# Optimization experiments

Hardware: AMD Instinct MI355X
Metric: run time of the kernel (lower is better)

## Reference

```python
import jax, jax.numpy as jnp
import numpy as np

EPS = 1e-5  # BatchNorm eps


def _conv_bn_tanh(h, w, b, g, be, m, v):
    # 3x3 conv, stride 1, SAME padding (pad = k//2), NCHW / OIHW
    y = jax.lax.conv_general_dilated(
        h, w, window_strides=(1, 1), padding='SAME',
        dimension_numbers=('NCHW', 'OIHW', 'NCHW'))
    y = y + b[None, :, None, None]
    # BatchNorm inference: gamma * (y - mean) / sqrt(var + eps) + beta
    scale = g * jax.lax.rsqrt(v + EPS)
    y = y * scale[None, :, None, None] + (be - m * scale)[None, :, None, None]
    return jnp.tanh(y)


def _unfold3x3(x):
    # torch F.unfold(k=3, pad=1, stride=1) -> (N, C, 9, H, W), kernel positions row-major
    N, C, H, W = x.shape
    xp = jnp.pad(x, ((0, 0), (0, 0), (1, 1), (1, 1)))
    patches = [xp[:, :, i:i + H, j:j + W] for i in range(3) for j in range(3)]
    return jnp.stack(patches, axis=2)  # (N, C, 9, H, W)


def setup_inputs() -> dict:
    key = jax.random.key(0)
    ks = jax.random.split(key, 24)
    N, C, H, W = 8, 64, 128, 128
    INTER, FEAT, NB, KK = 64, 6, 6, 9
    d = {}
    d['x'] = jax.random.normal(ks[0], (N, C, H, W), jnp.float32)
    d['w0'] = jax.random.normal(ks[1], (INTER, C, 3, 3), jnp.float32) * 0.05
    d['b0'] = jax.random.normal(ks[2], (INTER,), jnp.float32) * 0.05
    d['g0'] = jax.random.uniform(ks[3], (INTER,), jnp.float32)
    d['be0'] = jax.random.normal(ks[4], (INTER,), jnp.float32) * 0.05
    d['m0'] = jax.random.normal(ks[5], (INTER,), jnp.float32) * 0.05
    d['v0'] = jax.random.uniform(ks[6], (INTER,), jnp.float32)
    d['wm'] = jax.random.normal(ks[7], (5, INTER, INTER, 3, 3), jnp.float32) * 0.05
    d['bm'] = jax.random.normal(ks[8], (5, INTER), jnp.float32) * 0.05
    d['gm'] = jax.random.uniform(ks[9], (5, INTER), jnp.float32)
    d['bem'] = jax.random.normal(ks[10], (5, INTER), jnp.float32) * 0.05
    d['mm'] = jax.random.normal(ks[11], (5, INTER), jnp.float32) * 0.05
    d['vm'] = jax.random.uniform(ks[12], (5, INTER), jnp.float32)
    OC = FEAT * NB  # 36
    d['wl'] = jax.random.normal(ks[13], (OC, INTER, 3, 3), jnp.float32) * 0.05
    d['bl'] = jax.random.normal(ks[14], (OC,), jnp.float32) * 0.05
    d['gl'] = jax.random.uniform(ks[15], (OC,), jnp.float32)
    d['bel'] = jax.random.normal(ks[16], (OC,), jnp.float32) * 0.05
    d['ml'] = jax.random.normal(ks[17], (OC,), jnp.float32) * 0.05
    d['vl'] = jax.random.uniform(ks[18], (OC,), jnp.float32)
    d['bases'] = jax.random.normal(ks[19], (NB, KK), jnp.float32)  # FB bases buffer (6, 9)
    return d


def reference(x, w0, b0, g0, be0, m0, v0, wm, bm, gm, bem, mm, vm,
              wl, bl, gl, bel, ml, vl, bases):
    N, C, H, W = x.shape
    FEAT, NB = 6, 6
    # bases_net: conv-bn-tanh x7 (eval mode, dropout no-ops)
    h = _conv_bn_tanh(x, w0, b0, g0, be0, m0, v0)
    for i in range(5):
        h = _conv_bn_tanh(h, wm[i], bm[i], gm[i], bem[i], mm[i], vm[i])
    h = _conv_bn_tanh(h, wl, bl, gl, bel, ml, vl)  # (N, 36, H, W)
    bfeat = h.reshape(N, FEAT, NB, H, W)
    # per-pixel basis coefficients: (N, M, 9, H, W)
    bcoef = jnp.einsum('bmkhw,kl->bmlhw', bfeat, bases)
    patches = _unfold3x3(x)  # (N, C, 9, H, W)
    # dynamic conv: combine per-pixel coeffs with unfolded input
    out = jnp.einsum('bmlhw,bclhw->bcmhw', bcoef, patches)  # (N, C, M, H, W)
    return out.reshape(N, C * NB, H, W)
```

## Files before the change

kernel.cpp:

```cpp
#include <hip/hip_runtime.h>
#include <hip/hip_bf16.h>

typedef short bf16x4 __attribute__((ext_vector_type(4)));
typedef short bf16x8 __attribute__((ext_vector_type(8)));
typedef float f32x4  __attribute__((ext_vector_type(4)));

__device__ inline unsigned short f2us(float f) {
    __hip_bfloat16 h = __float2bfloat16(f);
    return *(unsigned short*)&h;
}
__device__ inline float us2f(unsigned short u) {
    union { unsigned int i; float f; } c; c.i = ((unsigned int)u) << 16; return c.f;
}
__device__ inline float tanh_fast(float x) {
    float xs = fminf(fmaxf(x, -20.f), 20.f);
    float t = __expf(2.f * xs);
    return 1.f - 2.f / (t + 1.f);
}

__global__ __launch_bounds__(256) void prep_x(const float* __restrict__ x,
                                              unsigned short* __restrict__ xcl)
{
    __shared__ unsigned short t2[128 * 68];
    int bid = blockIdx.x;
    int n = bid >> 7, h = bid & 127;
    const float* xp = x + (size_t)n * 64 * 16384 + h * 128;
    int t = threadIdx.x;
    for (int i = t; i < 8192; i += 256) {
        int ci = i >> 7, w = i & 127;
        t2[w * 68 + ci] = f2us(xp[(size_t)ci * 16384 + w]);
    }
    __syncthreads();
    unsigned short* op = xcl + ((size_t)(n * 16384 + h * 128)) * 64;
    for (int i = t; i < 1024; i += 256) {
        int w = i >> 3, c8 = i & 7;
        union { bf16x4 v[2]; uint4 q; } u;
        u.v[0] = *(bf16x4*)&t2[w * 68 + c8 * 8];
        u.v[1] = *(bf16x4*)&t2[w * 68 + c8 * 8 + 4];
        *(uint4*)(op + w * 64 + c8 * 8) = u.q;
    }
}

__global__ void prep_wf(const float* __restrict__ w0, const float* __restrict__ wm,
                        const float* __restrict__ wl, unsigned short* __restrict__ Wf)
{
    int idx = blockIdx.x * 256 + threadIdx.x;
    if (idx >= 258048) return;
    int l = idx / 36864, r = idx - l * 36864;
    int tp = r >> 12, r2 = r & 4095;
    int hh = r2 >> 11, nb = (r2 >> 9) & 3, ln = (r2 >> 3) & 63, j = r2 & 7;
    int ci = hh * 32 + (ln >> 4) * 8 + j;
    int co = nb * 16 + (ln & 15);
    float val = 0.f;
    if (l < 6) {
        const float* src = (l == 0) ? w0 : (wm + (size_t)(l - 1) * 36864);
        val = src[(co * 64 + ci) * 9 + tp];
    } else if (co < 36) {
        val = wl[(co * 64 + ci) * 9 + tp];
    }
    Wf[idx] = f2us(val);
}

__global__ void prep_ab(const float* b0, const float* g0, const float* be0,
                        const float* m0, const float* v0,
                        const float* bm, const float* gm, const float* bem,
                        const float* mm, const float* vm,
                        const float* bl, const float* gl, const float* bel,
                        const float* ml, const float* vl,
                        float* __restrict__ Af, float* __restrict__ Bf)
{
    int idx = blockIdx.x * 256 + threadIdx.x;
    if (idx >= 448) return;
    int l = idx >> 6, c = idx & 63;
    float b, g, be, m, v;
    if (l == 0) {
        b = b0[c]; g = g0[c]; be = be0[c]; m = m0[c]; v = v0[c];
    } else if (l < 6) {
        int o = (l - 1) * 64 + c;
        b = bm[o]; g = gm[o]; be = bem[o]; m = mm[o]; v = vm[o];
    } else {
        if (c >= 36) { Af[idx] = 0.f; Bf[idx] = 0.f; return; }
        b = bl[c]; g = gl[c]; be = bel[c]; m = ml[c]; v = vl[c];
    }
    float s = g / sqrtf(v + 1e-5f);
    Af[idx] = s;
    Bf[idx] = (b - m) * s + be;
}

__global__ __launch_bounds__(256)
void conv_mfma(const unsigned short* __restrict__ src,
               const unsigned short* __restrict__ Wf,
               const float* __restrict__ A, const float* __restrict__ B,
               unsigned short* __restrict__ dst)
{
    __shared__ unsigned short tile[18 * 18 * 68];
    const int n = blockIdx.z;
    const int h0 = blockIdx.y * 16, w0 = blockIdx.x * 16;
    const int t = threadIdx.x;
    const size_t ibase = (size_t)n * 16384 * 64;

    for (int i = t; i < 5184; i += 256) {
        int p = i >> 4, c4 = i & 15;
        int ty = p / 18, tx = p - ty * 18;
        int gy = h0 + ty - 1, gx = w0 + tx - 1;
        uint2 v = make_uint2(0u, 0u);
        if ((unsigned)gy < 128u && (unsigned)gx < 128u)
            v = *(const uint2*)(src + ibase + (size_t)(gy * 128 + gx) * 64 + c4 * 4);
        *(uint2*)&tile[p * 68 + c4 * 4] = v;
    }
    __syncthreads();

    const int ln = t & 63, wv = t >> 6;
    const int xln = ln & 15, qd = ln >> 4;

    f32x4 acc[4][4];
#pragma unroll
    for (int mt = 0; mt < 4; ++mt)
#pragma unroll
        for (int nb = 0; nb < 4; ++nb)
            acc[mt][nb] = (f32x4){0.f, 0.f, 0.f, 0.f};

    const uint4* wf4 = (const uint4*)Wf;
#pragma unroll
    for (int tp = 0; tp < 9; ++tp) {
        const int ky = tp / 3, kx = tp % 3;
        bf16x8 b[2][4];
#pragma unroll
        for (int hh = 0; hh < 2; ++hh)
#pragma unroll
            for (int nb = 0; nb < 4; ++nb) {
                uint4 q = wf4[((tp * 2 + hh) * 4 + nb) * 64 + ln];
                b[hh][nb] = *(bf16x8*)&q;
            }
#pragma unroll
        for (int mt = 0; mt < 4; ++mt) {
            const int off0 = ((wv * 4 + mt + ky) * 18 + xln + kx) * 68 + qd * 8;
#pragma unroll
            for (int hh = 0; hh < 2; ++hh) {
                union { bf16x8 v8; bf16x4 v4[2]; } a;
                a.v4[0] = *(const bf16x4*)&tile[off0 + hh * 32];
                a.v4[1] = *(const bf16x4*)&tile[off0 + hh * 32 + 4];
#pragma unroll
                for (int nb = 0; nb < 4; ++nb)
                    acc[mt][nb] = __builtin_amdgcn_mfma_f32_16x16x32_bf16(
                        a.v8, b[hh][nb], acc[mt][nb], 0, 0, 0);
            }
        }
    }

#pragma unroll
    for (int mt = 0; mt < 4; ++mt) {
        const int gy = h0 + wv * 4 + mt;
        unsigned short* dp = dst + ibase + (size_t)(gy * 128) * 64;
#pragma unroll
        for (int nb = 0; nb < 4; ++nb) {
            const int co = nb * 16 + xln;
            const float As = A[co], Bs = B[co];
#pragma unroll
            for (int r = 0; r < 4; ++r) {
                const int gx = w0 + qd * 4 + r;
                float y = tanh_fast(fmaf(acc[mt][nb][r], As, Bs));
                dp[(size_t)gx * 64 + co] = f2us(y);
            }
        }
    }
}

__global__ __launch_bounds__(256)
void dyn_conv(const float* __restrict__ x, const unsigned short* __restrict__ h7,
              const float* __restrict__ bases, float* __restrict__ out)
{
    __shared__ float tile[32 * 10 * 34];
    const int n = blockIdx.z;
    const int h0 = blockIdx.y * 8, w0 = blockIdx.x * 32;
    const float* xp = x + (size_t)n * 64 * 16384;
    const int t = threadIdx.x;
    const int tw = t & 31, th = t >> 5;
    const int h = h0 + th, w = w0 + tw;

    float bs[54];
#pragma unroll
    for (int i = 0; i < 54; ++i) bs[i] = bases[i];

    union { uint4 q[5]; unsigned short s[40]; } hv;
    const unsigned short* hp = h7 + (size_t)(n * 16384 + h * 128 + w) * 64;
#pragma unroll
    for (int i = 0; i < 5; ++i) hv.q[i] = ((const uint4*)hp)[i];

    float coef[54];
#pragma unroll
    for (int i = 0; i < 54; ++i) coef[i] = 0.f;
#pragma unroll
    for (int m = 0; m < 6; ++m)
#pragma unroll
        for (int k = 0; k < 6; ++k) {
            float f = us2f(hv.s[m * 6 + k]);
#pragma unroll
            for (int l = 0; l < 9; ++l)
                coef[m * 9 + l] = fmaf(f, bs[k * 9 + l], coef[m * 9 + l]);
        }

    float* op = out + (size_t)n * 384 * 16384 + h * 128 + w;

    for (int half = 0; half < 2; ++half) {
        if (half) __syncthreads();
        for (int idx = t; idx < 32 * 340; idx += 256) {
            int ci = idx / 340, r = idx % 340, y = r / 34, xw = r % 34;
            int gy = h0 + y - 1, gx = w0 + xw - 1;
            float v = 0.f;
            if ((unsigned)gy < 128u && (unsigned)gx < 128u)
                v = xp[(size_t)(half * 32 + ci) * 16384 + gy * 128 + gx];
            tile[idx] = v;
        }
        __syncthreads();

#pragma unroll 1
        for (int c = 0; c < 32; ++c) {
            float xv[9];
#pragma unroll
            for (int ky = 0; ky < 3; ++ky)
#pragma unroll
                for (int kx = 0; kx < 3; ++kx)
                    xv[ky * 3 + kx] = tile[c * 340 + (th + ky) * 34 + (tw + kx)];
            int cg = half * 32 + c;
#pragma unroll
            for (int m = 0; m < 6; ++m) {
                float s = 0.f;
#pragma unroll
                for (int l = 0; l < 9; ++l) s = fmaf(coef[m * 9 + l], xv[l], s);
                op[(size_t)(cg * 6 + m) * 16384] = s;
            }
        }
    }
}

extern "C" void kernel_launch(void* const* d_in, const int* in_sizes, int n_in,
                              void* d_out, int out_size, void* d_ws, size_t ws_size,
                              hipStream_t stream)
{
    const float* x   = (const float*)d_in[0];
    const float* w0  = (const float*)d_in[1];
    const float* b0  = (const float*)d_in[2];
    const float* g0  = (const float*)d_in[3];
    const float* be0 = (const float*)d_in[4];
    const float* m0  = (const float*)d_in[5];
    const float* v0  = (const float*)d_in[6];
    const float* wm  = (const float*)d_in[7];
    const float* bm  = (const float*)d_in[8];
    const float* gm  = (const float*)d_in[9];
    const float* bem = (const float*)d_in[10];
    const float* mm  = (const float*)d_in[11];
    const float* vm  = (const float*)d_in[12];
    const float* wl  = (const float*)d_in[13];
    const float* bl  = (const float*)d_in[14];
    const float* gl  = (const float*)d_in[15];
    const float* bel = (const float*)d_in[16];
    const float* ml  = (const float*)d_in[17];
    const float* vl  = (const float*)d_in[18];
    const float* bas = (const float*)d_in[19];

    unsigned short* Wfb = (unsigned short*)d_ws;
    float* Af  = (float*)((char*)d_ws + 524288);
    float* Bf  = Af + 448;
    unsigned short* xcl  = (unsigned short*)((char*)d_ws + (size_t)(2  << 20));
    unsigned short* bufA = (unsigned short*)((char*)d_ws + (size_t)(2  << 20) + 16777216);
    unsigned short* bufB = (unsigned short*)((char*)d_ws + (size_t)(2  << 20) + 2 * 16777216);

    prep_x<<<1024, 256, 0, stream>>>(x, xcl);
    prep_wf<<<1008, 256, 0, stream>>>(w0, wm, wl, Wfb);
    prep_ab<<<2, 256, 0, stream>>>(b0, g0, be0, m0, v0,
                                   bm, gm, bem, mm, vm,
                                   bl, gl, bel, ml, vl, Af, Bf);

    dim3 cg(8, 8, 8);
    conv_mfma<<<cg, 256, 0, stream>>>(xcl,  Wfb + 0 * 36864, Af + 0,   Bf + 0,   bufA);
    conv_mfma<<<cg, 256, 0, stream>>>(bufA, Wfb + 1 * 36864, Af + 64,  Bf + 64,  bufB);
    conv_mfma<<<cg, 256, 0, stream>>>(bufB, Wfb + 2 * 36864, Af + 128, Bf + 128, bufA);
    conv_mfma<<<cg, 256, 0, stream>>>(bufA, Wfb + 3 * 36864, Af + 192, Bf + 192, bufB);
    conv_mfma<<<cg, 256, 0, stream>>>(bufB, Wfb + 4 * 36864, Af + 256, Bf + 256, bufA);
    conv_mfma<<<cg, 256, 0, stream>>>(bufA, Wfb + 5 * 36864, Af + 320, Bf + 320, bufB);
    conv_mfma<<<cg, 256, 0, stream>>>(bufB, Wfb + 6 * 36864, Af + 384, Bf + 384, bufA);

    dim3 dg(4, 16, 8);
    dyn_conv<<<dg, 256, 0, stream>>>(x, bufA, bas, (float*)d_out);
}
```

Before: 500.7 us.

## Stage conv tiles and weights in LDS via direct global-to-LDS loads

The conv kernel now runs 512-thread blocks on 16x32 output tiles. The haloed input tile and all 3x3 weight fragments are copied straight from global memory into LDS with global_load_lds, using an XOR swizzle on the channel chunks to avoid bank conflicts. This replaces per-thread register-staged tile loads and repeated global weight reads, and the wider tile gives each block more output work. In exchange it uses about 152KB of LDS per block, which limits residency to one block per CU, and it adds a zero-fill pass before the loads.

```diff
diff --git a/kernel.cpp b/kernel.cpp
--- a/kernel.cpp
+++ b/kernel.cpp
@@ -16,6 +16,13 @@
     float xs = fminf(fmaxf(x, -20.f), 20.f);
     float t = __expf(2.f * xs);
     return 1.f - 2.f / (t + 1.f);
+}
+
+__device__ inline void gload_lds16(const void* g, void* l) {
+    __builtin_amdgcn_global_load_lds(
+        (const __attribute__((address_space(1))) void*)g,
+        (__attribute__((address_space(3))) void*)l,
+        16, 0, 0);
 }
 
 __global__ __launch_bounds__(256) void prep_x(const float* __restrict__ x,
@@ -87,40 +94,56 @@
     Bf[idx] = (b - m) * s + be;
 }
 
-__global__ __launch_bounds__(256)
+#define LDS_W_OFF 78336
+__global__ __launch_bounds__(512, 2)
 void conv_mfma(const unsigned short* __restrict__ src,
                const unsigned short* __restrict__ Wf,
                const float* __restrict__ A, const float* __restrict__ B,
                unsigned short* __restrict__ dst)
 {
-    __shared__ unsigned short tile[18 * 18 * 68];
+    __shared__ __align__(16) unsigned char smem[152064];
     const int n = blockIdx.z;
-    const int h0 = blockIdx.y * 16, w0 = blockIdx.x * 16;
+    const int h0 = blockIdx.y * 16, w0 = blockIdx.x * 32;
     const int t = threadIdx.x;
-    const size_t ibase = (size_t)n * 16384 * 64;
-
-    for (int i = t; i < 5184; i += 256) {
-        int p = i >> 4, c4 = i & 15;
-        int ty = p / 18, tx = p - ty * 18;
-        int gy = h0 + ty - 1, gx = w0 + tx - 1;
-        uint2 v = make_uint2(0u, 0u);
-        if ((unsigned)gy < 128u && (unsigned)gx < 128u)
-            v = *(const uint2*)(src + ibase + (size_t)(gy * 128 + gx) * 64 + c4 * 4);
-        *(uint2*)&tile[p * 68 + c4 * 4] = v;
-    }
-    __syncthreads();
-
     const int ln = t & 63, wv = t >> 6;
     const int xln = ln & 15, qd = ln >> 4;
-
-    f32x4 acc[4][4];
-#pragma unroll
-    for (int mt = 0; mt < 4; ++mt)
-#pragma unroll
-        for (int nb = 0; nb < 4; ++nb)
-            acc[mt][nb] = (f32x4){0.f, 0.f, 0.f, 0.f};
-
-    const uint4* wf4 = (const uint4*)Wf;
+    const size_t ibase = (size_t)n * 16384 * 64;
+
+    {
+        uint4 z = make_uint4(0u, 0u, 0u, 0u);
+        for (int c = t; c < 4896; c += 512)
+            *(uint4*)(smem + (size_t)c * 16) = z;
+    }
+    __syncthreads();
+
+    const unsigned short* srcn = src + ibase;
+    for (int i = wv; i < 77; i += 8) {
+        int g = i * 64 + ln;
+        int p = g >> 3, jj = g & 7;
+        int ty = (p * 1928) >> 16;
+        int tx = p - ty * 34;
+        int gy = h0 + ty - 1, gx = w0 + tx - 1;
+        int js = jj ^ (p & 7);
+        bool ok = (g < 4896) & ((unsigned)gy < 128u) & ((unsigned)gx < 128u);
+        const unsigned short* gsrc = srcn + (ptrdiff_t)(gy * 128 + gx) * 64 + js * 8;
+        if (ok) gload_lds16(gsrc, smem + (size_t)i * 1024);
+    }
+    for (int i = wv; i < 72; i += 8) {
+        const unsigned short* gsrc = Wf + ((size_t)(i * 64 + ln)) * 8;
+        gload_lds16(gsrc, smem + LDS_W_OFF + (size_t)i * 1024);
+    }
+    __syncthreads();
+
+    f32x4 acc[2][2][4];
+#pragma unroll
+    for (int rh = 0; rh < 2; ++rh)
+#pragma unroll
+        for (int hf = 0; hf < 2; ++hf)
+#pragma unroll
+            for (int nb = 0; nb < 4; ++nb)
+                acc[rh][hf][nb] = (f32x4){0.f, 0.f, 0.f, 0.f};
+
+    const int rbase = wv * 2;
 #pragma unroll
     for (int tp = 0; tp < 9; ++tp) {
         const int ky = tp / 3, kx = tp % 3;
@@ -128,39 +151,44 @@
 #pragma unroll
         for (int hh = 0; hh < 2; ++hh)
 #pragma unroll
-            for (int nb = 0; nb < 4; ++nb) {
-                uint4 q = wf4[((tp * 2 + hh) * 4 + nb) * 64 + ln];
-                b[hh][nb] = *(bf16x8*)&q;
+            for (int nb = 0; nb < 4; ++nb)
+                b[hh][nb] = *(const bf16x8*)(smem + LDS_W_OFF +
+                    (((((tp * 2 + hh) * 4 + nb) * 64) + ln) << 4));
+#pragma unroll
+        for (int rh = 0; rh < 2; ++rh) {
+#pragma unroll
+            for (int hf = 0; hf < 2; ++hf) {
+                const int p = (rbase + rh + ky) * 34 + hf * 16 + xln + kx;
+                const int pb = p * 128, sw = (p & 7) << 4;
+#pragma unroll
+                for (int hh = 0; hh < 2; ++hh) {
+                    bf16x8 a = *(const bf16x8*)(smem + pb +
+                                                (((qd + 4 * hh) << 4) ^ sw));
+#pragma unroll
+                    for (int nb = 0; nb < 4; ++nb)
+                        acc[rh][hf][nb] = __builtin_amdgcn_mfma_f32_16x16x32_bf16(
+                            a, b[hh][nb], acc[rh][hf][nb], 0, 0, 0);
+                }
             }
-#pragma unroll
-        for (int mt = 0; mt < 4; ++mt) {
-            const int off0 = ((wv * 4 + mt + ky) * 18 + xln + kx) * 68 + qd * 8;
-#pragma unroll
-            for (int hh = 0; hh < 2; ++hh) {
-                union { bf16x8 v8; bf16x4 v4[2]; } a;
-                a.v4[0] = *(const bf16x4*)&tile[off0 + hh * 32];
-                a.v4[1] = *(const bf16x4*)&tile[off0 + hh * 32 + 4];
-#pragma unroll
-                for (int nb = 0; nb < 4; ++nb)
-                    acc[mt][nb] = __builtin_amdgcn_mfma_f32_16x16x32_bf16(
-                        a.v8, b[hh][nb], acc[mt][nb], 0, 0, 0);
-            }
-        }
-    }
-
-#pragma unroll
-    for (int mt = 0; mt < 4; ++mt) {
-        const int gy = h0 + wv * 4 + mt;
-        unsigned short* dp = dst + ibase + (size_t)(gy * 128) * 64;
-#pragma unroll
-        for (int nb = 0; nb < 4; ++nb) {
-            const int co = nb * 16 + xln;
-            const float As = A[co], Bs = B[co];
-#pragma unroll
-            for (int r = 0; r < 4; ++r) {
-                const int gx = w0 + qd * 4 + r;
-                float y = tanh_fast(fmaf(acc[mt][nb][r], As, Bs));
-                dp[(size_t)gx * 64 + co] = f2us(y);
+        }
+    }
+
+#pragma unroll
+    for (int nb = 0; nb < 4; ++nb) {
+        const int co = nb * 16 + xln;
+        const float As = A[co], Bs = B[co];
+#pragma unroll
+        for (int rh = 0; rh < 2; ++rh) {
+            const int gy = h0 + rbase + rh;
+            unsigned short* dp = dst + ibase + (size_t)(gy * 128) * 64;
+#pragma unroll
+            for (int hf = 0; hf < 2; ++hf) {
+#pragma unroll
+                for (int r = 0; r < 4; ++r) {
+                    const int gx = w0 + hf * 16 + qd * 4 + r;
+                    float y = tanh_fast(fmaf(acc[rh][hf][nb][r], As, Bs));
+                    dp[(size_t)gx * 64 + co] = f2us(y);
+                }
             }
         }
     }
@@ -272,14 +300,14 @@
                                    bm, gm, bem, mm, vm,
                                    bl, gl, bel, ml, vl, Af, Bf);
 
-    dim3 cg(8, 8, 8);
-    conv_mfma<<<cg, 256, 0, stream>>>(xcl,  Wfb + 0 * 36864, Af + 0,   Bf + 0,   bufA);
-    conv_mfma<<<cg, 256, 0, stream>>>(bufA, Wfb + 1 * 36864, Af + 64,  Bf + 64,  bufB);
-    conv_mfma<<<cg, 256, 0, stream>>>(bufB, Wfb + 2 * 36864, Af + 128, Bf + 128, bufA);
-    conv_mfma<<<cg, 256, 0, stream>>>(bufA, Wfb + 3 * 36864, Af + 192, Bf + 192, bufB);
-    conv_mfma<<<cg, 256, 0, stream>>>(bufB, Wfb + 4 * 36864, Af + 256, Bf + 256, bufA);
-    conv_mfma<<<cg, 256, 0, stream>>>(bufA, Wfb + 5 * 36864, Af + 320, Bf + 320, bufB);
-    conv_mfma<<<cg, 256, 0, stream>>>(bufB, Wfb + 6 * 36864, Af + 384, Bf + 384, bufA);
+    dim3 cg(4, 8, 8);
+    conv_mfma<<<cg, 512, 0, stream>>>(xcl,  Wfb + 0 * 36864, Af + 0,   Bf + 0,   bufA);
+    conv_mfma<<<cg, 512, 0, stream>>>(bufA, Wfb + 1 * 36864, Af + 64,  Bf + 64,  bufB);
+    conv_mfma<<<cg, 512, 0, stream>>>(bufB, Wfb + 2 * 36864, Af + 128, Bf + 128, bufA);
+    conv_mfma<<<cg, 512, 0, stream>>>(bufA, Wfb + 3 * 36864, Af + 192, Bf + 192, bufB);
+    conv_mfma<<<cg, 512, 0, stream>>>(bufB, Wfb + 4 * 36864, Af + 256, Bf + 256, bufA);
+    conv_mfma<<<cg, 512, 0, stream>>>(bufA, Wfb + 5 * 36864, Af + 320, Bf + 320, bufB);
+    conv_mfma<<<cg, 512, 0, stream>>>(bufB, Wfb + 6 * 36864, Af + 384, Bf + 384, bufA);
 
     dim3 dg(4, 16, 8);
     dyn_conv<<<dg, 256, 0, stream>>>(x, bufA, bas, (float*)d_out);
```

Measured after the change: 413.2 us. 1.21x faster.
